# Performance work log

Hardware: AMD Instinct MI355X
Metric: run time of the kernel (lower is better)

Reference implementation:

```python
import jax, jax.numpy as jnp
import numpy as np

B, T, N, H = 512, 128, 128, 256


def setup_inputs() -> dict:
    key = jax.random.key(0)
    ks = jax.random.split(key, 8)
    rn = lambda k, shape, sc: (jax.random.normal(k, shape, jnp.float32) * sc)
    return {
        "data": rn(ks[0], (B, T, N), 1.0),
        "h0": jnp.zeros((B, H), jnp.float32),
        # SimpleRNNCell params: h_t = tanh(x@Wx + h@Wh + b)
        "Wx": rn(ks[1], (N, H), 0.05),
        "Wh": rn(ks[2], (H, H), 0.05),
        "b": jnp.zeros((H,), jnp.float32),
        # InputAttention: w1: Dense(T) over last dim T; w2: Dense(T) over hidden; v: Dense(1)
        "W1": rn(ks[3], (T, T), 0.05),
        "b1": jnp.zeros((T,), jnp.float32),
        "W2": rn(ks[4], (H, T), 0.05),
        "b2": jnp.zeros((T,), jnp.float32),
        "Wv": rn(ks[5], (T, 1), 0.05),
        "bv": jnp.zeros((1,), jnp.float32),
        "n": N,
    }


def reference(data, h0, Wx, Wh, b, W1, b1, W2, b2, Wv, bv, n):
    # data: (B, T, n); h0: (B, H)
    Tlen = data.shape[1]
    x_perm = jnp.swapaxes(data, 1, 2)          # (B, n, T) == Permute((2,1))(x)
    pre = x_perm @ W1 + b1                      # w1(x_perm): loop-invariant, hoisted

    def step(h, x_t):
        # SimpleRNNCell: new state used for this step's attention
        h_new = jnp.tanh(x_t @ Wx + h @ Wh + b)                 # (B, H)
        q = h_new @ W2 + b2                                      # w2(RepeatVector(n)(h)) per row -> (B, T)
        score = jnp.tanh(pre + q[:, None, :])                    # (B, n, T)
        e = score @ Wv + bv                                      # (B, n, 1)
        e = jnp.swapaxes(e, 1, 2)                                # Permute((2,1)) -> (B, 1, n)
        alpha = jax.nn.softmax(e, axis=-1)                       # softmax over n
        return h_new, alpha

    xs = jnp.swapaxes(data, 0, 1)               # (T, B, n): data[:, t, :] per step
    _, alphas = jax.lax.scan(step, h0, xs)      # (T, B, 1, n)
    # faithful to tf.reshape(alpha_seq.stack(), (-1, T, n))
    alpha_seq = alphas.reshape(-1, Tlen, n)     # (B, T, n)
    return data * alpha_seq
```

## Files before the change

kernel.cpp:

```cpp
#include <hip/hip_runtime.h>


#define C2L 2.8853900817779268f
#define L2E 1.4426950408889634f

typedef _Float16 hf;
typedef _Float16 hf4 __attribute__((ext_vector_type(4)));
typedef _Float16 hf8 __attribute__((ext_vector_type(8)));
typedef float f32x4 __attribute__((ext_vector_type(4)));

__device__ __forceinline__ float fast_exp2(float x){
#if __has_builtin(__builtin_amdgcn_exp2f)
  return __builtin_amdgcn_exp2f(x);
#else
  return exp2f(x);
#endif
}
__device__ __forceinline__ float fast_rcp(float x){
#if __has_builtin(__builtin_amdgcn_rcpf)
  return __builtin_amdgcn_rcpf(x);
#else
  return 1.f/x;
#endif
}

__global__ __launch_bounds__(256) void k_prep_w(const float* __restrict__ Wx,
    const float* __restrict__ W2, const float* __restrict__ W1,
    hf* __restrict__ wts){
  int tid = blockIdx.x*256 + threadIdx.x;
  if (tid < 32768){
    int n = tid >> 7, k = tid & 127;
    wts[tid] = (hf)Wx[k*256 + n];
  } else if (tid < 65536){
    int t2 = tid - 32768;
    int n = t2 >> 8, k = t2 & 255;
    wts[tid] = (hf)W2[k*128 + n];
  } else {
    int t3 = tid - 65536;
    int n = t3 >> 7, k = t3 & 127;
    wts[tid] = (hf)W1[k*128 + n];
  }
}

template<int K, int MODE>
__global__ __launch_bounds__(256) void k_gemm(const void* __restrict__ Asrc,
    const hf* __restrict__ Bt, const float* __restrict__ bias,
    float* __restrict__ Cout){
  constexpr int SA = 136;
  __shared__ alignas(16) hf As[64*SA];
  __shared__ alignas(16) hf Bs[128*SA];
  const int tid = threadIdx.x;
  const int w = tid >> 6, lane = tid & 63;
  const int c = lane & 15, q = lane >> 4;
  const int bx = blockIdx.x;
  const int col0 = (MODE==0) ? blockIdx.y*128 : 0;

  float br[8];
  #pragma unroll
  for (int ni=0; ni<8; ni++) br[ni] = bias[col0 + ni*16 + c];

  f32x4 acc[8];
  #pragma unroll
  for (int ni=0; ni<8; ni++) acc[ni] = (f32x4){0.f,0.f,0.f,0.f};

  for (int kc=0; kc<K/128; kc++){
    if (MODE == 0){
      const float* A = (const float*)Asrc + (long)bx*64*128;
      #pragma unroll
      for (int v=0; v<8; v++){
        int f4 = v*256 + tid;
        int m = f4 >> 5, k4 = (f4 & 31)*4;
        float4 d = *(const float4*)&A[m*128 + k4];
        hf4 h = {(hf)d.x,(hf)d.y,(hf)d.z,(hf)d.w};
        *(hf4*)&As[m*SA + k4] = h;
      }
    } else if (MODE == 1){
      const hf* A = (const hf*)Asrc + (long)bx*64*256;
      #pragma unroll
      for (int v=0; v<4; v++){
        int f8 = v*256 + tid;
        int m = f8 >> 4, k8 = (f8 & 15)*8;
        *(hf8*)&As[m*SA + k8] = *(const hf8*)&A[m*256 + kc*128 + k8];
      }
    } else {
      const float* A = (const float*)Asrc + (long)(bx>>1)*16384;
      const int i0 = (bx & 1)*64;
      #pragma unroll
      for (int v=0; v<8; v++){
        int f4 = v*256 + tid;
        int t = f4 >> 4, i4 = (f4 & 15)*4;
        float4 d = *(const float4*)&A[t*128 + i0 + i4];
        As[(i4+0)*SA + t] = (hf)d.x;
        As[(i4+1)*SA + t] = (hf)d.y;
        As[(i4+2)*SA + t] = (hf)d.z;
        As[(i4+3)*SA + t] = (hf)d.w;
      }
    }
    #pragma unroll
    for (int v=0; v<8; v++){
      int f8 = v*256 + tid;
      int n = f8 >> 4, k8 = (f8 & 15)*8;
      *(hf8*)&Bs[n*SA + k8] = *(const hf8*)&Bt[(col0+n)*K + kc*128 + k8];
    }
    __syncthreads();
    #pragma unroll
    for (int kk=0; kk<4; kk++){
      hf8 a = *(const hf8*)&As[(w*16 + c)*SA + kk*32 + q*8];
      #pragma unroll
      for (int ni=0; ni<8; ni++){
        hf8 b = *(const hf8*)&Bs[(ni*16 + c)*SA + kk*32 + q*8];
        acc[ni] = __builtin_amdgcn_mfma_f32_16x16x32_f16(a, b, acc[ni], 0, 0, 0);
      }
    }
    __syncthreads();
  }
  #pragma unroll
  for (int ni=0; ni<8; ni++){
    #pragma unroll
    for (int r=0; r<4; r++){
      int rloc = w*16 + q*4 + r;
      int col = col0 + ni*16 + c;
      float val = acc[ni][r] + br[ni];
      int addr;
      if (MODE == 0){
        int R = bx*64 + rloc;
        int b_ = R >> 7, t_ = R & 127;
        addr = (t_*512 + b_)*256 + col;
      } else if (MODE == 1){
        int R = bx*64 + rloc;
        addr = R*128 + col;
        val = fast_exp2(C2L*val);
      } else {
        int b_ = bx >> 1, i_ = (bx & 1)*64 + rloc;
        addr = b_*16384 + i_*128 + col;
        val = fast_exp2(C2L*val);
      }
      Cout[addr] = val;
    }
  }
}

__global__ __launch_bounds__(1024, 4) void k_rnn(const float* __restrict__ h0,
    const float* __restrict__ Wh, const float* __restrict__ xw,
    hf* __restrict__ Hb){
  __shared__ alignas(16) char hs[2*8192];
  const int tid = threadIdx.x;
  const int w = tid >> 6, lane = tid & 63;
  const int c = lane & 15, q = lane >> 4;
  const int b0 = blockIdx.x * 16;
  const int oc0 = w*16 + 4*q;
  hf8 aw[8];
  #pragma unroll
  for (int kc=0; kc<8; kc++){
    #pragma unroll
    for (int e=0; e<8; e++){
      aw[kc][e] = (hf)Wh[(kc*32 + q*8 + e)*256 + w*16 + c];
    }
  }
  if (tid < 512){
    int m = tid >> 5, s8 = tid & 31;
    const float* src = &h0[(b0 + m)*256 + s8*8];
    float4 d0 = *(const float4*)&src[0];
    float4 d1 = *(const float4*)&src[4];
    hf8 hv = {(hf)d0.x,(hf)d0.y,(hf)d0.z,(hf)d0.w,
              (hf)d1.x,(hf)d1.y,(hf)d1.z,(hf)d1.w};
    *(hf8*)&hs[m*512 + ((s8 ^ (m & 7)) << 4)] = hv;
  }
  float4 xA = *(const float4*)&xw[(0*512 + b0 + c)*256 + oc0];
  float4 xB = *(const float4*)&xw[(1*512 + b0 + c)*256 + oc0];
  __syncthreads();
  #pragma unroll 1
  for (int t=0; t<128; t+=2){
    #pragma unroll
    for (int half=0; half<2; half++){
      const int T = t + half;
      const int p = T & 1;
      hf8 hb[8];
      #pragma unroll
      for (int kc=0; kc<8; kc++)
        hb[kc] = *(const hf8*)&hs[p*8192 + c*512
                                  + ((((kc<<2)|q) ^ (c & 7)) << 4)];
      f32x4 al = (f32x4){0.f,0.f,0.f,0.f}, ah = al;
      #pragma unroll
      for (int kc=0; kc<4; kc++){
        al = __builtin_amdgcn_mfma_f32_16x16x32_f16(aw[kc],   hb[kc],   al,0,0,0);
        ah = __builtin_amdgcn_mfma_f32_16x16x32_f16(aw[kc+4], hb[kc+4], ah,0,0,0);
      }
      float4 nv = (T+2 < 128)
        ? *(const float4*)&xw[((T+2)*512 + b0 + c)*256 + oc0]
        : (float4){0.f,0.f,0.f,0.f};
      {
        float4 xv = half ? xB : xA;
        float v0 = al[0] + ah[0] + xv.x;
        float v1 = al[1] + ah[1] + xv.y;
        float v2 = al[2] + ah[2] + xv.z;
        float v3 = al[3] + ah[3] + xv.w;
        float ea = fast_exp2(v0*C2L) + 1.f;
        float eb = fast_exp2(v1*C2L) + 1.f;
        float R0 = fast_rcp(ea*eb);
        float ec = fast_exp2(v2*C2L) + 1.f;
        float ed = fast_exp2(v3*C2L) + 1.f;
        float R1 = fast_rcp(ec*ed);
        hf4 h4 = {(hf)fmaf(-2.f*eb, R0, 1.f), (hf)fmaf(-2.f*ea, R0, 1.f),
                  (hf)fmaf(-2.f*ed, R1, 1.f), (hf)fmaf(-2.f*ec, R1, 1.f)};
        *(hf4*)&hs[(p^1)*8192 + c*512
                   + (((oc0 >> 3) ^ (c & 7)) << 4) + (oc0 & 7)*2] = h4;
        *(hf4*)&Hb[(T*512 + b0 + c)*256 + oc0] = h4;
        if (half) xB = nv; else xA = nv;
      }
      asm volatile("s_waitcnt lgkmcnt(0)\n\ts_barrier" ::: "memory");
    }
  }
}

__global__ __launch_bounds__(512, 4) void k_attn(const float* __restrict__ P,
    const float* __restrict__ Qm, const float* __restrict__ Wv,
    const float* __restrict__ data, float* __restrict__ out){
  __shared__ alignas(16) float qs[32*128];
  __shared__ alignas(16) float wvs[128];
  __shared__ alignas(16) float epart[2][4][4][128];
  __shared__ float red[2][4][2];
  const int b = blockIdx.x, tile = blockIdx.y;
  const int tid = threadIdx.x;
  const int i = tid & 127, g = tid >> 7;
  const int t0 = tile*32;
  if (tid < 128) wvs[tid] = -2.f*Wv[tid];
  #pragma unroll
  for (int v=0; v<2; v++){
    int flat = v*2048 + tid*4;
    int tt = flat >> 7, c = flat & 127;
    *(float4*)&qs[flat] = *(const float4*)&Qm[((t0+tt)*512 + b)*128 + c];
  }
  float4 p4[8];
  const float* prow = P + b*16384 + i*128 + g*32;
  #pragma unroll
  for (int v=0; v<8; v++) p4[v] = *(const float4*)&prow[v*4];
  __syncthreads();
  for (int tp=0; tp<8; tp++){
    const int pp = tp & 1;
    const float* qb  = &qs[(4*tp)*128 + g*32];
    const float* wvr = &wvs[g*32];
    float acc0=0.f, acc1=0.f, acc2=0.f, acc3=0.f;
    #pragma unroll
    for (int mm=0; mm<8; mm++){
      float4 Pv = p4[mm];
      float4 wv = *(const float4*)&wvr[mm*4];
      #pragma unroll
      for (int tl=0; tl<4; tl++){
        float4 qq = *(const float4*)&qb[tl*128 + mm*4];
        float u = fmaf(Pv.x, qq.x, 1.f), v = fmaf(Pv.y, qq.y, 1.f);
        float x = fmaf(Pv.z, qq.z, 1.f), y = fmaf(Pv.w, qq.w, 1.f);
        float d01 = u*v, d23 = x*y;
        float n01 = fmaf(wv.x, v, wv.y*u);
        float n23 = fmaf(wv.z, y, wv.w*x);
        float N = fmaf(n01, d23, n23*d01);
        float r = fast_rcp(d01*d23);
        float term = N*r;
        if (tl==0) acc0 += term;
        else if (tl==1) acc1 += term;
        else if (tl==2) acc2 += term;
        else acc3 += term;
      }
    }
    epart[pp][g][0][i] = acc0;
    epart[pp][g][1][i] = acc1;
    epart[pp][g][2][i] = acc2;
    epart[pp][g][3][i] = acc3;
    __syncthreads();
    float e = epart[pp][0][g][i] + epart[pp][1][g][i]
            + epart[pp][2][g][i] + epart[pp][3][g][i];
    float pe = fast_exp2(e*L2E);
    float sm = pe;
    #pragma unroll
    for (int off=32; off; off>>=1) sm += __shfl_xor(sm, off);
    if ((tid & 63) == 0) red[pp][g][(tid>>6)&1] = sm;
    __syncthreads();
    float ssum = red[pp][g][0] + red[pp][g][1];
    float alpha = pe * fast_rcp(ssum);
    int t = t0 + 4*tp + g;
    int base = (t*512 + b)*128 + i;
    out[base] = data[base]*alpha;
  }
}

extern "C" void kernel_launch(void* const* d_in, const int* in_sizes, int n_in,
                              void* d_out, int out_size, void* d_ws, size_t ws_size,
                              hipStream_t stream) {
  const float* data = (const float*)d_in[0];
  const float* h0   = (const float*)d_in[1];
  const float* Wx   = (const float*)d_in[2];
  const float* Wh   = (const float*)d_in[3];
  const float* bb   = (const float*)d_in[4];
  const float* W1   = (const float*)d_in[5];
  const float* b1   = (const float*)d_in[6];
  const float* W2   = (const float*)d_in[7];
  const float* b2   = (const float*)d_in[8];
  const float* Wv   = (const float*)d_in[9];
  float* wsp = (float*)d_ws;
  float* P   = wsp;
  float* xwQ = wsp + 8388608;
  hf*    Hbf = (hf*)(wsp + 25165824);
  hf*    wts = (hf*)(wsp + 33554432);
  const hf* Wxt = wts;
  const hf* W2t = wts + 32768;
  const hf* W1t = wts + 65536;
  float* out = (float*)d_out;

  hipLaunchKernelGGL(k_prep_w, dim3(320), dim3(256), 0, stream, Wx, W2, W1, wts);
  hipLaunchKernelGGL((k_gemm<128,0>), dim3(1024,2), dim3(256), 0, stream,
                     (const void*)data, Wxt, bb, xwQ);
  hipLaunchKernelGGL((k_gemm<128,2>), dim3(1024),   dim3(256), 0, stream,
                     (const void*)data, W1t, b1, P);
  hipLaunchKernelGGL(k_rnn, dim3(32), dim3(1024), 0, stream, h0, Wh, xwQ, Hbf);
  hipLaunchKernelGGL((k_gemm<256,1>), dim3(1024),   dim3(256), 0, stream,
                     (const void*)Hbf, W2t, b2, xwQ);
  hipLaunchKernelGGL(k_attn, dim3(512, 4), dim3(512), 0, stream, P, xwQ, Wv, data, out);
}
```

Before: 336.9 us.

## Fuse W2 projection into attention kernel and store x@Wx in fp16

Removes the separate K=256 GEMM that computed exp(2*(h@W2+b2)). Each attention block now stages its 32 hidden-state rows in LDS, runs the small MFMA projection itself and writes the exponentiated q values into LDS, which saves one launch and a round trip of the fp32 Q matrix through global memory. The x@Wx intermediate is also stored as fp16 instead of fp32, halving that buffer's traffic into the serial RNN kernel at some cost in precision. The attention kernel now does extra MFMA work and W2t loads per block, and the LDS staging area is reused for both hidden states and q.

```diff
diff --git a/kernel.cpp b/kernel.cpp
--- a/kernel.cpp
+++ b/kernel.cpp
@@ -22,6 +22,10 @@
 #else
   return 1.f/x;
 #endif
+}
+__device__ __forceinline__ float4 ld4h(const hf* p){
+  hf4 h = *(const hf4*)p;
+  return (float4){(float)h.x, (float)h.y, (float)h.z, (float)h.w};
 }
 
 __global__ __launch_bounds__(256) void k_prep_w(const float* __restrict__ Wx,
@@ -42,10 +46,10 @@
   }
 }
 
-template<int K, int MODE>
+template<int MODE>
 __global__ __launch_bounds__(256) void k_gemm(const void* __restrict__ Asrc,
     const hf* __restrict__ Bt, const float* __restrict__ bias,
-    float* __restrict__ Cout){
+    void* __restrict__ Cout){
   constexpr int SA = 136;
   __shared__ alignas(16) hf As[64*SA];
   __shared__ alignas(16) hf Bs[128*SA];
@@ -63,56 +67,45 @@
   #pragma unroll
   for (int ni=0; ni<8; ni++) acc[ni] = (f32x4){0.f,0.f,0.f,0.f};
 
-  for (int kc=0; kc<K/128; kc++){
-    if (MODE == 0){
-      const float* A = (const float*)Asrc + (long)bx*64*128;
-      #pragma unroll
-      for (int v=0; v<8; v++){
-        int f4 = v*256 + tid;
-        int m = f4 >> 5, k4 = (f4 & 31)*4;
-        float4 d = *(const float4*)&A[m*128 + k4];
-        hf4 h = {(hf)d.x,(hf)d.y,(hf)d.z,(hf)d.w};
-        *(hf4*)&As[m*SA + k4] = h;
-      }
-    } else if (MODE == 1){
-      const hf* A = (const hf*)Asrc + (long)bx*64*256;
-      #pragma unroll
-      for (int v=0; v<4; v++){
-        int f8 = v*256 + tid;
-        int m = f8 >> 4, k8 = (f8 & 15)*8;
-        *(hf8*)&As[m*SA + k8] = *(const hf8*)&A[m*256 + kc*128 + k8];
-      }
-    } else {
-      const float* A = (const float*)Asrc + (long)(bx>>1)*16384;
-      const int i0 = (bx & 1)*64;
-      #pragma unroll
-      for (int v=0; v<8; v++){
-        int f4 = v*256 + tid;
-        int t = f4 >> 4, i4 = (f4 & 15)*4;
-        float4 d = *(const float4*)&A[t*128 + i0 + i4];
-        As[(i4+0)*SA + t] = (hf)d.x;
-        As[(i4+1)*SA + t] = (hf)d.y;
-        As[(i4+2)*SA + t] = (hf)d.z;
-        As[(i4+3)*SA + t] = (hf)d.w;
-      }
-    }
+  if (MODE == 0){
+    const float* A = (const float*)Asrc + (long)bx*64*128;
     #pragma unroll
     for (int v=0; v<8; v++){
-      int f8 = v*256 + tid;
-      int n = f8 >> 4, k8 = (f8 & 15)*8;
-      *(hf8*)&Bs[n*SA + k8] = *(const hf8*)&Bt[(col0+n)*K + kc*128 + k8];
-    }
-    __syncthreads();
-    #pragma unroll
-    for (int kk=0; kk<4; kk++){
-      hf8 a = *(const hf8*)&As[(w*16 + c)*SA + kk*32 + q*8];
-      #pragma unroll
-      for (int ni=0; ni<8; ni++){
-        hf8 b = *(const hf8*)&Bs[(ni*16 + c)*SA + kk*32 + q*8];
-        acc[ni] = __builtin_amdgcn_mfma_f32_16x16x32_f16(a, b, acc[ni], 0, 0, 0);
-      }
-    }
-    __syncthreads();
+      int f4 = v*256 + tid;
+      int m = f4 >> 5, k4 = (f4 & 31)*4;
+      float4 d = *(const float4*)&A[m*128 + k4];
+      hf4 h = {(hf)d.x,(hf)d.y,(hf)d.z,(hf)d.w};
+      *(hf4*)&As[m*SA + k4] = h;
+    }
+  } else {
+    const float* A = (const float*)Asrc + (long)(bx>>1)*16384;
+    const int i0 = (bx & 1)*64;
+    #pragma unroll
+    for (int v=0; v<8; v++){
+      int f4 = v*256 + tid;
+      int t = f4 >> 4, i4 = (f4 & 15)*4;
+      float4 d = *(const float4*)&A[t*128 + i0 + i4];
+      As[(i4+0)*SA + t] = (hf)d.x;
+      As[(i4+1)*SA + t] = (hf)d.y;
+      As[(i4+2)*SA + t] = (hf)d.z;
+      As[(i4+3)*SA + t] = (hf)d.w;
+    }
+  }
+  #pragma unroll
+  for (int v=0; v<8; v++){
+    int f8 = v*256 + tid;
+    int n = f8 >> 4, k8 = (f8 & 15)*8;
+    *(hf8*)&Bs[n*SA + k8] = *(const hf8*)&Bt[(col0+n)*128 + k8];
+  }
+  __syncthreads();
+  #pragma unroll
+  for (int kk=0; kk<4; kk++){
+    hf8 a = *(const hf8*)&As[(w*16 + c)*SA + kk*32 + q*8];
+    #pragma unroll
+    for (int ni=0; ni<8; ni++){
+      hf8 b = *(const hf8*)&Bs[(ni*16 + c)*SA + kk*32 + q*8];
+      acc[ni] = __builtin_amdgcn_mfma_f32_16x16x32_f16(a, b, acc[ni], 0, 0, 0);
+    }
   }
   #pragma unroll
   for (int ni=0; ni<8; ni++){
@@ -121,27 +114,20 @@
       int rloc = w*16 + q*4 + r;
       int col = col0 + ni*16 + c;
       float val = acc[ni][r] + br[ni];
-      int addr;
       if (MODE == 0){
         int R = bx*64 + rloc;
         int b_ = R >> 7, t_ = R & 127;
-        addr = (t_*512 + b_)*256 + col;
-      } else if (MODE == 1){
-        int R = bx*64 + rloc;
-        addr = R*128 + col;
-        val = fast_exp2(C2L*val);
+        ((hf*)Cout)[(t_*512 + b_)*256 + col] = (hf)val;
       } else {
         int b_ = bx >> 1, i_ = (bx & 1)*64 + rloc;
-        addr = b_*16384 + i_*128 + col;
-        val = fast_exp2(C2L*val);
+        ((float*)Cout)[b_*16384 + i_*128 + col] = fast_exp2(C2L*val);
       }
-      Cout[addr] = val;
     }
   }
 }
 
 __global__ __launch_bounds__(1024, 4) void k_rnn(const float* __restrict__ h0,
-    const float* __restrict__ Wh, const float* __restrict__ xw,
+    const float* __restrict__ Wh, const hf* __restrict__ xw,
     hf* __restrict__ Hb){
   __shared__ alignas(16) char hs[2*8192];
   const int tid = threadIdx.x;
@@ -166,8 +152,8 @@
               (hf)d1.x,(hf)d1.y,(hf)d1.z,(hf)d1.w};
     *(hf8*)&hs[m*512 + ((s8 ^ (m & 7)) << 4)] = hv;
   }
-  float4 xA = *(const float4*)&xw[(0*512 + b0 + c)*256 + oc0];
-  float4 xB = *(const float4*)&xw[(1*512 + b0 + c)*256 + oc0];
+  float4 xA = ld4h(&xw[(0*512 + b0 + c)*256 + oc0]);
+  float4 xB = ld4h(&xw[(1*512 + b0 + c)*256 + oc0]);
   __syncthreads();
   #pragma unroll 1
   for (int t=0; t<128; t+=2){
@@ -187,7 +173,7 @@
         ah = __builtin_amdgcn_mfma_f32_16x16x32_f16(aw[kc+4], hb[kc+4], ah,0,0,0);
       }
       float4 nv = (T+2 < 128)
-        ? *(const float4*)&xw[((T+2)*512 + b0 + c)*256 + oc0]
+        ? ld4h(&xw[((T+2)*512 + b0 + c)*256 + oc0])
         : (float4){0.f,0.f,0.f,0.f};
       {
         float4 xv = half ? xB : xA;
@@ -214,27 +200,60 @@
 }
 
 __global__ __launch_bounds__(512, 4) void k_attn(const float* __restrict__ P,
-    const float* __restrict__ Qm, const float* __restrict__ Wv,
+    const hf* __restrict__ Hbf, const hf* __restrict__ W2t,
+    const float* __restrict__ b2, const float* __restrict__ Wv,
     const float* __restrict__ data, float* __restrict__ out){
-  __shared__ alignas(16) float qs[32*128];
+  __shared__ alignas(16) char u0[32*264*2];
   __shared__ alignas(16) float wvs[128];
   __shared__ alignas(16) float epart[2][4][4][128];
   __shared__ float red[2][4][2];
+  hf* hstage = (hf*)u0;
+  float* qs = (float*)u0;
   const int b = blockIdx.x, tile = blockIdx.y;
   const int tid = threadIdx.x;
   const int i = tid & 127, g = tid >> 7;
+  const int lane = tid & 63, wvid = tid >> 6;
+  const int c16 = lane & 15, q4 = lane >> 4;
   const int t0 = tile*32;
+  #pragma unroll
+  for (int v=0; v<2; v++){
+    int ch = v*512 + tid;
+    int row = ch >> 5, k8 = (ch & 31)*8;
+    *(hf8*)&hstage[row*264 + k8] =
+        *(const hf8*)&Hbf[((long)(t0+row)*512 + b)*256 + k8];
+  }
   if (tid < 128) wvs[tid] = -2.f*Wv[tid];
-  #pragma unroll
-  for (int v=0; v<2; v++){
-    int flat = v*2048 + tid*4;
-    int tt = flat >> 7, c = flat & 127;
-    *(float4*)&qs[flat] = *(const float4*)&Qm[((t0+tt)*512 + b)*128 + c];
-  }
   float4 p4[8];
   const float* prow = P + b*16384 + i*128 + g*32;
   #pragma unroll
   for (int v=0; v<8; v++) p4[v] = *(const float4*)&prow[v*4];
+  __syncthreads();
+  f32x4 sacc[2];
+  #pragma unroll
+  for (int hh=0; hh<2; hh++){
+    const int n0 = (wvid>>1)*32 + hh*16;
+    f32x4 accq = (f32x4){0.f,0.f,0.f,0.f};
+    #pragma unroll
+    for (int kc=0; kc<8; kc++){
+      hf8 a = *(const hf8*)&hstage[((wvid&1)*16 + c16)*264 + kc*32 + q4*8];
+      hf8 bf = *(const hf8*)&W2t[(n0 + c16)*256 + kc*32 + q4*8];
+      accq = __builtin_amdgcn_mfma_f32_16x16x32_f16(a, bf, accq, 0,0,0);
+    }
+    sacc[hh] = accq;
+  }
+  float bb0 = b2[(wvid>>1)*32 + c16];
+  float bb1 = b2[(wvid>>1)*32 + 16 + c16];
+  __syncthreads();
+  #pragma unroll
+  for (int hh=0; hh<2; hh++){
+    const int n0 = (wvid>>1)*32 + hh*16;
+    const float bb = hh ? bb1 : bb0;
+    #pragma unroll
+    for (int r=0; r<4; r++){
+      int row = (wvid&1)*16 + q4*4 + r;
+      qs[row*128 + n0 + c16] = fast_exp2(C2L*(sacc[hh][r] + bb));
+    }
+  }
   __syncthreads();
   for (int tp=0; tp<8; tp++){
     const int pp = tp & 1;
@@ -298,7 +317,7 @@
   const float* Wv   = (const float*)d_in[9];
   float* wsp = (float*)d_ws;
   float* P   = wsp;
-  float* xwQ = wsp + 8388608;
+  hf*    xwh = (hf*)(wsp + 8388608);
   hf*    Hbf = (hf*)(wsp + 25165824);
   hf*    wts = (hf*)(wsp + 33554432);
   const hf* Wxt = wts;
@@ -307,12 +326,11 @@
   float* out = (float*)d_out;
 
   hipLaunchKernelGGL(k_prep_w, dim3(320), dim3(256), 0, stream, Wx, W2, W1, wts);
-  hipLaunchKernelGGL((k_gemm<128,0>), dim3(1024,2), dim3(256), 0, stream,
-                     (const void*)data, Wxt, bb, xwQ);
-  hipLaunchKernelGGL((k_gemm<128,2>), dim3(1024),   dim3(256), 0, stream,
-                     (const void*)data, W1t, b1, P);
-  hipLaunchKernelGGL(k_rnn, dim3(32), dim3(1024), 0, stream, h0, Wh, xwQ, Hbf);
-  hipLaunchKernelGGL((k_gemm<256,1>), dim3(1024),   dim3(256), 0, stream,
-                     (const void*)Hbf, W2t, b2, xwQ);
-  hipLaunchKernelGGL(k_attn, dim3(512, 4), dim3(512), 0, stream, P, xwQ, Wv, data, out);
-}
+  hipLaunchKernelGGL((k_gemm<0>), dim3(1024,2), dim3(256), 0, stream,
+                     (const void*)data, Wxt, bb, (void*)xwh);
+  hipLaunchKernelGGL((k_gemm<2>), dim3(1024),   dim3(256), 0, stream,
+                     (const void*)data, W1t, b1, (void*)P);
+  hipLaunchKernelGGL(k_rnn, dim3(32), dim3(1024), 0, stream, h0, Wh, xwh, Hbf);
+  hipLaunchKernelGGL(k_attn, dim3(512, 4), dim3(512), 0, stream,
+                     P, Hbf, W2t, b2, Wv, data, out);
+}
```

Measured after the change: 385.4 us. 1.14x slower.
